# Kernel tuning notes

Hardware: AMD Instinct MI355X
Metric: run time of the kernel (lower is better)

Reference implementation:

```python
import jax, jax.numpy as jnp
import numpy as np

B, T, I = 64, 512, 64
H, O = 256, 64
S, D = 128, 128  # memory_slots == memory_dim (required by the module's update broadcast)


def setup_inputs() -> dict:
    key = jax.random.key(0)
    ks = jax.random.split(key, 12)
    s_ih = 1.0 / np.sqrt(H)
    return {
        "x_seq": jax.random.normal(ks[0], (B, T, I), dtype=jnp.float32),
        # LSTMCell params (torch layout: [4H, I]/[4H, H], gate order i,f,g,o)
        "W_ih": jax.random.uniform(ks[1], (4 * H, I), minval=-s_ih, maxval=s_ih),
        "W_hh": jax.random.uniform(ks[2], (4 * H, H), minval=-s_ih, maxval=s_ih),
        "b_ih": jax.random.uniform(ks[3], (4 * H,), minval=-s_ih, maxval=s_ih),
        "b_hh": jax.random.uniform(ks[4], (4 * H,), minval=-s_ih, maxval=s_ih),
        "W_read": jax.random.normal(ks[5], (D, H)) * 0.02,
        "b_read": jnp.zeros((D,), jnp.float32),
        "W_write": jax.random.normal(ks[6], (D, H)) * 0.02,
        "b_write": jnp.zeros((D,), jnp.float32),
        "W_dec": jax.random.normal(ks[7], (O, H + D)) * 0.02,
        "b_dec": jnpp if False else jnp.zeros((O,), jnp.float32),
    }


def reference(x_seq, W_ih, W_hh, b_ih, b_hh, W_read, b_read, W_write, b_write, W_dec, b_dec):
    def step(carry, x):
        h, c, mem = carry  # h,c: [B,H]; mem: [B,S,D]
        gates = x @ W_ih.T + b_ih + h @ W_hh.T + b_hh  # [B,4H]
        i_g, f_g, g_g, o_g = jnp.split(gates, 4, axis=-1)
        c = jax.nn.sigmoid(f_g) * c + jax.nn.sigmoid(i_g) * jnp.tanh(g_g)
        h = jax.nn.sigmoid(o_g) * jnp.tanh(c)
        # read addressing
        read_keys = h @ W_read.T + b_read                      # [B,D]
        rw = jax.nn.softmax(jnp.einsum('bsd,bd->bs', mem, read_keys), axis=1)
        read_vec = jnp.einsum('bs,bsd->bd', rw, mem)           # [B,D]
        # write addressing + update (add vector = tanh(logits), S == D)
        write_keys = h @ W_write.T + b_write                   # [B,D]
        lw = jnp.einsum('bsd,bd->bs', mem, write_keys)         # [B,S]
        ww = jax.nn.softmax(lw, axis=1)
        add = jnp.tanh(lw)                                     # [B,S] == [B,D]
        mem = mem * (1.0 - ww[:, :, None]) + ww[:, :, None] * add[:, None, :]
        out = jnp.concatenate([h, read_vec], axis=-1) @ W_dec.T + b_dec  # [B,O]
        return (h, c, mem), out

    h0 = jnp.zeros((B, H), x_seq.dtype)
    c0 = jnp.zeros((B, H), x_seq.dtype)
    mem0 = jnp.zeros((B, S, D), x_seq.dtype)  # zero-init buffer, batched after first write
    _, outs = jax.lax.scan(step, (h0, c0, mem0), jnp.swapaxes(x_seq, 0, 1))
    return jnp.swapaxes(outs, 0, 1)  # [B,T,O]
```

## Files before the change

kernel.cpp:

```cpp
#include <hip/hip_runtime.h>


typedef _Float16 f16x2 __attribute__((ext_vector_type(2)));

#define NB   64
#define TT   512
#define RPP  100
#define QRG  25
#define QLD  7
#define XP_BYTES  (67108864u)
#define HD_BYTES  (16777216u)

__device__ unsigned char g_ntm_ws[XP_BYTES + HD_BYTES];

union U32H { unsigned int u; f16x2 h; };
union USH  { _Float16 f; unsigned short u; };
static __device__ __forceinline__ unsigned int pack2f(float a, float b) {
    U32H v; v.h = f16x2{(_Float16)a, (_Float16)b}; return v.u;
}
static __device__ __forceinline__ f16x2 up(unsigned int u) { U32H v; v.u = u; return v.h; }
static __device__ __forceinline__ unsigned short f2s(float a) { USH v; v.f = (_Float16)a; return v.u; }

__device__ __forceinline__ float sigf(float x) { return 1.0f / (1.0f + __expf(-x)); }
__device__ __forceinline__ float tanhfast(float x) {
    float e = __expf(2.0f * x);
    return 1.0f - 2.0f / (e + 1.0f);
}

#if __has_builtin(__builtin_amdgcn_fdot2)
__device__ __forceinline__ float dot2(f16x2 a, f16x2 b, float c) {
    return __builtin_amdgcn_fdot2(a, b, c, false);
}
#else
__device__ __forceinline__ float dot2(f16x2 a, f16x2 b, float c) {
    return c + (float)a.x * (float)b.x + (float)a.y * (float)b.y;
}
#endif

__global__ void __attribute__((amdgpu_flat_work_group_size(512, 512)))
xproj_kernel(const float* __restrict__ x_seq, const float* __restrict__ W_ih,
             const float* __restrict__ b_ih, const float* __restrict__ b_hh,
             unsigned short* XPh)
{
    if (!XPh) XPh = (unsigned short*)g_ntm_ws;
    __shared__ unsigned int xq[128 * 32];
    const int tid = threadIdx.x;
    const int b   = blockIdx.x >> 2;
    const int q   = blockIdx.x & 3;

    {
        const float* src = x_seq + ((size_t)b * TT + (size_t)q * 128 + (tid >> 2)) * 64
                         + (tid & 3) * 16;
        unsigned int* dst = xq + (tid >> 2) * 32 + (tid & 3) * 8;
#pragma unroll
        for (int i = 0; i < 4; ++i) {
            float4 v = ((const float4*)src)[i];
            dst[2 * i]     = pack2f(v.x, v.y);
            dst[2 * i + 1] = pack2f(v.z, v.w);
        }
    }

    unsigned int w0p[32], w1p[32];
    {
        const float* r0 = W_ih + (size_t)tid * 64;
        const float* r1 = W_ih + (size_t)(tid + 512) * 64;
#pragma unroll
        for (int i = 0; i < 16; ++i) {
            float4 v0 = *(const float4*)(r0 + 4 * i);
            float4 v1 = *(const float4*)(r1 + 4 * i);
            w0p[2*i] = pack2f(v0.x, v0.y); w0p[2*i+1] = pack2f(v0.z, v0.w);
            w1p[2*i] = pack2f(v1.x, v1.y); w1p[2*i+1] = pack2f(v1.z, v1.w);
        }
    }
    const float bias0 = b_ih[tid]       + b_hh[tid];
    const float bias1 = b_ih[tid + 512] + b_hh[tid + 512];
    const int   g4A   = (tid & 255) * 4 + ((tid < 256) ? 0 : 1);
    __syncthreads();

    unsigned short* outh = XPh + ((size_t)b * TT + (size_t)q * 128) * 1024;
    for (int tt = 0; tt < 128; ++tt) {
        const uint4* xr = (const uint4*)(xq + tt * 32);
        float a0 = bias0, a1 = bias1;
        float a2 = 0.f, a3 = 0.f, a4 = 0.f, a5 = 0.f, a6 = 0.f, a7 = 0.f;
#pragma unroll
        for (int i = 0; i < 8; ++i) {
            uint4 xv = xr[i];
            a0 = dot2(up(w0p[4*i]),   up(xv.x), a0);  a1 = dot2(up(w1p[4*i]),   up(xv.x), a1);
            a2 = dot2(up(w0p[4*i+1]), up(xv.y), a2);  a3 = dot2(up(w1p[4*i+1]), up(xv.y), a3);
            a4 = dot2(up(w0p[4*i+2]), up(xv.z), a4);  a5 = dot2(up(w1p[4*i+2]), up(xv.z), a5);
            a6 = dot2(up(w0p[4*i+3]), up(xv.w), a6);  a7 = dot2(up(w1p[4*i+3]), up(xv.w), a7);
        }
        const float gA = (a0 + a2) + (a4 + a6);
        const float gB = (a1 + a3) + (a5 + a7);
        outh[tt * 1024 + g4A]     = f2s(gA);
        outh[tt * 1024 + g4A + 2] = f2s(gB);
    }
}

__global__ void
__attribute__((amdgpu_flat_work_group_size(512, 512), amdgpu_waves_per_eu(2, 2),
               amdgpu_num_vgpr(240)))
ntm_rec(const float* __restrict__ W_hh,
        const unsigned short* __restrict__ XPh_in,
        unsigned short* __restrict__ Hd_in)
{
    extern __shared__ char smem[];
    uint4*    wl4 = (uint4*)smem;
    _Float16* h16 = (_Float16*)(smem + 14 * 512 * 16);

    const unsigned short* XPh = XPh_in ? XPh_in : (const unsigned short*)g_ntm_ws;
    unsigned short*       Hd  = Hd_in  ? Hd_in  : (unsigned short*)(g_ntm_ws + XP_BYTES);

    const int tid = threadIdx.x;
    const int b   = blockIdx.x;
    const int u   = tid >> 1;
    const int e   = tid & 1;

    const float* r0 = W_hh + (size_t)(u + 512 * e) * 256;
    const float* r1 = W_hh + (size_t)(256 + u + 512 * e) * 256;

    f16x2 w0[RPP], w1[RPP];
#pragma unroll
    for (int p = 0; p < RPP; ++p) {
        float2 va = *(const float2*)(r0 + 2 * p);
        float2 vb = *(const float2*)(r1 + 2 * p);
        w0[p] = f16x2{(_Float16)va.x, (_Float16)va.y};
        w1[p] = f16x2{(_Float16)vb.x, (_Float16)vb.y};
    }
#pragma unroll
    for (int qq = 0; qq < QLD; ++qq) {
        const float* s0 = r0 + 2 * (RPP + 4 * qq);
        const float* s1 = r1 + 2 * (RPP + 4 * qq);
        wl4[(2 * qq)     * 512 + tid] = make_uint4(pack2f(s0[0], s0[1]), pack2f(s0[2], s0[3]),
                                                   pack2f(s0[4], s0[5]), pack2f(s0[6], s0[7]));
        wl4[(2 * qq + 1) * 512 + tid] = make_uint4(pack2f(s1[0], s1[1]), pack2f(s1[2], s1[3]),
                                                   pack2f(s1[4], s1[5]), pack2f(s1[6], s1[7]));
    }
    if (tid < 64) ((uint4*)h16)[tid] = make_uint4(0u, 0u, 0u, 0u);
    float c_state = 0.f;
    __syncthreads();

    const unsigned int* xpb = (const unsigned int*)XPh + (size_t)b * TT * 512;
    uint4*              Hd4 = (uint4*)Hd + (size_t)b * TT * 32;

    unsigned int xpc = xpb[tid];

    for (int t = 0; t < TT; ++t) {
        const uint4* hq = (const uint4*)(h16 + (t & 1) * 256);
        unsigned int xpn = xpc;
        if (t + 1 < TT) xpn = xpb[(size_t)(t + 1) * 512 + tid];

        float a0 = 0.f, a1 = 0.f, a2 = 0.f, a3 = 0.f;
#pragma unroll
        for (int q = 0; q < QRG; ++q) {
            const uint4 hv = hq[q];
            a0 = dot2(w0[4*q],   up(hv.x), a0);  a2 = dot2(w1[4*q],   up(hv.x), a2);
            a1 = dot2(w0[4*q+1], up(hv.y), a1);  a3 = dot2(w1[4*q+1], up(hv.y), a3);
            a0 = dot2(w0[4*q+2], up(hv.z), a0);  a2 = dot2(w1[4*q+2], up(hv.z), a2);
            a1 = dot2(w0[4*q+3], up(hv.w), a1);  a3 = dot2(w1[4*q+3], up(hv.w), a3);
        }
#pragma unroll
        for (int qq = 0; qq < QLD; ++qq) {
            const uint4 hv = hq[QRG + qq];
            const uint4 wv0 = wl4[(2 * qq)     * 512 + tid];
            const uint4 wv1 = wl4[(2 * qq + 1) * 512 + tid];
            a0 = dot2(up(wv0.x), up(hv.x), a0);  a2 = dot2(up(wv1.x), up(hv.x), a2);
            a1 = dot2(up(wv0.y), up(hv.y), a1);  a3 = dot2(up(wv1.y), up(hv.y), a3);
            a0 = dot2(up(wv0.z), up(hv.z), a0);  a2 = dot2(up(wv1.z), up(hv.z), a2);
            a1 = dot2(up(wv0.w), up(hv.w), a1);  a3 = dot2(up(wv1.w), up(hv.w), a3);
        }
        const f16x2 xg = up(xpc);
        const float gM0 = (a0 + a1) + (float)xg.x;
        const float gM1 = (a2 + a3) + (float)xg.y;
        const float p0 = __shfl_xor(gM0, 1);
        const float p1 = __shfl_xor(gM1, 1);
        const float gi = e ? p0 : gM0;
        const float gf = e ? p1 : gM1;
        const float gg = e ? gM0 : p0;
        const float go = e ? gM1 : p1;
        c_state = sigf(gf) * c_state + sigf(gi) * tanhfast(gg);
        const float hn = sigf(go) * tanhfast(c_state);

        _Float16* hw = h16 + ((t + 1) & 1) * 256;
        if (!e) hw[u] = (_Float16)hn;
        __syncthreads();
        if (tid < 32) Hd4[(size_t)t * 32 + tid] = ((const uint4*)hw)[tid];
        xpc = xpn;
    }
}

__global__ void __attribute__((amdgpu_flat_work_group_size(256, 256)))
dec_kernel(const unsigned short* __restrict__ Hd_in,
           const float* __restrict__ W_dec, const float* __restrict__ b_dec,
           float* __restrict__ out)
{
    const unsigned short* Hd = Hd_in ? Hd_in : (const unsigned short*)(g_ntm_ws + XP_BYTES);
    __shared__ unsigned int wdl[64 * 132];
    __shared__ uint4 ht[32 * 32];

    const int tid = threadIdx.x;
    const int b = blockIdx.x >> 2, q = blockIdx.x & 3;

    for (int idx = tid; idx < 64 * 128; idx += 256) {
        const int o = idx >> 7, pp = idx & 127;
        wdl[o * 132 + pp] = pack2f(W_dec[(size_t)o * 384 + 2 * pp],
                                   W_dec[(size_t)o * 384 + 2 * pp + 1]);
    }
    const int o = tid & 63, tq = tid >> 6;
    const float bd = b_dec[o];
    const uint4* Hdb  = (const uint4*)Hd + ((size_t)b * TT + (size_t)q * 128) * 32;
    float*       outb = out + ((size_t)b * TT + (size_t)q * 128) * 64;

    for (int s = 0; s < 4; ++s) {
        __syncthreads();
#pragma unroll
        for (int i = 0; i < 4; ++i) {
            const int idx = tid + 256 * i;
            ht[idx] = Hdb[s * 1024 + idx];
        }
        __syncthreads();

        float acc[8];
#pragma unroll
        for (int j = 0; j < 8; ++j) acc[j] = 0.f;

#pragma unroll
        for (int c = 0; c < 8; ++c) {
            uint4 w0, w1, w2, w3;
            {
                const unsigned int* wp = wdl + o * 132 + 16 * c;
                w0 = make_uint4(wp[0],  wp[1],  wp[2],  wp[3]);
                w1 = make_uint4(wp[4],  wp[5],  wp[6],  wp[7]);
                w2 = make_uint4(wp[8],  wp[9],  wp[10], wp[11]);
                w3 = make_uint4(wp[12], wp[13], wp[14], wp[15]);
            }
#pragma unroll
            for (int j = 0; j < 8; ++j) {
                const uint4* hr = &ht[(tq * 8 + j) * 32 + 4 * c];
                const uint4 h0 = hr[0], h1 = hr[1], h2 = hr[2], h3 = hr[3];
                float d = acc[j];
                d = dot2(up(w0.x), up(h0.x), d); d = dot2(up(w0.y), up(h0.y), d);
                d = dot2(up(w0.z), up(h0.z), d); d = dot2(up(w0.w), up(h0.w), d);
                d = dot2(up(w1.x), up(h1.x), d); d = dot2(up(w1.y), up(h1.y), d);
                d = dot2(up(w1.z), up(h1.z), d); d = dot2(up(w1.w), up(h1.w), d);
                d = dot2(up(w2.x), up(h2.x), d); d = dot2(up(w2.y), up(h2.y), d);
                d = dot2(up(w2.z), up(h2.z), d); d = dot2(up(w2.w), up(h2.w), d);
                d = dot2(up(w3.x), up(h3.x), d); d = dot2(up(w3.y), up(h3.y), d);
                d = dot2(up(w3.z), up(h3.z), d); d = dot2(up(w3.w), up(h3.w), d);
                acc[j] = d;
            }
        }
#pragma unroll
        for (int j = 0; j < 8; ++j)
            outb[(size_t)(s * 32 + tq * 8 + j) * 64 + o] = acc[j] + bd;
    }
}

extern "C" void kernel_launch(void* const* d_in, const int* in_sizes, int n_in,
                              void* d_out, int out_size, void* d_ws, size_t ws_size,
                              hipStream_t stream) {
    const float* x_seq = (const float*)d_in[0];
    const float* W_ih  = (const float*)d_in[1];
    const float* W_hh  = (const float*)d_in[2];
    const float* b_ih  = (const float*)d_in[3];
    const float* b_hh  = (const float*)d_in[4];
    const float* W_dec = (const float*)d_in[9];
    const float* b_dec = (const float*)d_in[10];
    float* out = (float*)d_out;

    unsigned short* XPh = nullptr;
    unsigned short* Hd  = nullptr;
    if (ws_size >= (size_t)XP_BYTES + HD_BYTES) {
        XPh = (unsigned short*)d_ws;
        Hd  = (unsigned short*)((unsigned char*)d_ws + XP_BYTES);
    }

    hipLaunchKernelGGL(xproj_kernel, dim3(256), dim3(512), 0, stream,
                       x_seq, W_ih, b_ih, b_hh, XPh);

    const size_t smem_rec = (size_t)14 * 512 * 16 + 1024;
    hipFuncSetAttribute((const void*)&ntm_rec,
                        hipFuncAttributeMaxDynamicSharedMemorySize, (int)smem_rec);
    hipLaunchKernelGGL(ntm_rec, dim3(NB), dim3(512), smem_rec, stream,
                       W_hh, XPh, Hd);

    hipLaunchKernelGGL(dec_kernel, dim3(256), dim3(256), 0, stream,
                       Hd, W_dec, b_dec, out);
}
```

Before: 947.2 us.

## Split recurrent W_hh weights across VGPRs, LDS and AGPRs

The recurrent LSTM kernel now keeps 44 packed fp16 weight pairs per row in VGPRs, 36 in LDS and 48 in accumulation registers (AGPRs), written and read back with inline v_accvgpr instructions. Before, the split was 100 in VGPRs and 28 in LDS. The fixed VGPR cap is dropped. The aim is to reduce VGPR pressure and keep more weights resident per step, which cuts the LDS traffic of the per-timestep matvec. The cost is an extra accvgpr read for every AGPR-held weight each step, plus more LDS use.

New measurement: 1.233 ms. +30.2%, slower.

```diff
diff --git a/kernel.cpp b/kernel.cpp
--- a/kernel.cpp
+++ b/kernel.cpp
@@ -5,9 +5,11 @@
 
 #define NB   64
 #define TT   512
-#define RPP  100
-#define QRG  25
-#define QLD  7
+#define RREG 44
+#define QRG  11
+#define QLD  9
+#define QAG  12
+#define NAG  48
 #define XP_BYTES  (67108864u)
 #define HD_BYTES  (16777216u)
 
@@ -98,15 +100,14 @@
 }
 
 __global__ void
-__attribute__((amdgpu_flat_work_group_size(512, 512), amdgpu_waves_per_eu(2, 2),
-               amdgpu_num_vgpr(240)))
+__attribute__((amdgpu_flat_work_group_size(512, 512), amdgpu_waves_per_eu(2, 2)))
 ntm_rec(const float* __restrict__ W_hh,
         const unsigned short* __restrict__ XPh_in,
         unsigned short* __restrict__ Hd_in)
 {
     extern __shared__ char smem[];
     uint4*    wl4 = (uint4*)smem;
-    _Float16* h16 = (_Float16*)(smem + 14 * 512 * 16);
+    _Float16* h16 = (_Float16*)(smem + 18 * 512 * 16);
 
     const unsigned short* XPh = XPh_in ? XPh_in : (const unsigned short*)g_ntm_ws;
     unsigned short*       Hd  = Hd_in  ? Hd_in  : (unsigned short*)(g_ntm_ws + XP_BYTES);
@@ -119,23 +120,34 @@
     const float* r0 = W_hh + (size_t)(u + 512 * e) * 256;
     const float* r1 = W_hh + (size_t)(256 + u + 512 * e) * 256;
 
-    f16x2 w0[RPP], w1[RPP];
-#pragma unroll
-    for (int p = 0; p < RPP; ++p) {
+    f16x2 w0[RREG], w1[RREG];
+#pragma unroll
+    for (int p = 0; p < RREG; ++p) {
         float2 va = *(const float2*)(r0 + 2 * p);
         float2 vb = *(const float2*)(r1 + 2 * p);
         w0[p] = f16x2{(_Float16)va.x, (_Float16)va.y};
         w1[p] = f16x2{(_Float16)vb.x, (_Float16)vb.y};
     }
 #pragma unroll
-    for (int qq = 0; qq < QLD; ++qq) {
-        const float* s0 = r0 + 2 * (RPP + 4 * qq);
-        const float* s1 = r1 + 2 * (RPP + 4 * qq);
-        wl4[(2 * qq)     * 512 + tid] = make_uint4(pack2f(s0[0], s0[1]), pack2f(s0[2], s0[3]),
-                                                   pack2f(s0[4], s0[5]), pack2f(s0[6], s0[7]));
-        wl4[(2 * qq + 1) * 512 + tid] = make_uint4(pack2f(s1[0], s1[1]), pack2f(s1[2], s1[3]),
-                                                   pack2f(s1[4], s1[5]), pack2f(s1[6], s1[7]));
-    }
+    for (int j = 0; j < QLD; ++j) {
+        const float* s0 = r0 + 2 * (RREG + 4 * j);
+        const float* s1 = r1 + 2 * (RREG + 4 * j);
+        wl4[(2 * j)     * 512 + tid] = make_uint4(pack2f(s0[0], s0[1]), pack2f(s0[2], s0[3]),
+                                                  pack2f(s0[4], s0[5]), pack2f(s0[6], s0[7]));
+        wl4[(2 * j + 1) * 512 + tid] = make_uint4(pack2f(s1[0], s1[1]), pack2f(s1[2], s1[3]),
+                                                  pack2f(s1[4], s1[5]), pack2f(s1[6], s1[7]));
+    }
+    unsigned int wagA[NAG], wagB[NAG];
+#pragma unroll
+    for (int p = 0; p < NAG; ++p) {
+        const float* sA = r0 + 160 + 2 * p;
+        const float* sB = r1 + 160 + 2 * p;
+        unsigned int ua = pack2f(sA[0], sA[1]);
+        unsigned int ub = pack2f(sB[0], sB[1]);
+        asm volatile("v_accvgpr_write_b32 %0, %1" : "=a"(wagA[p]) : "v"(ua));
+        asm volatile("v_accvgpr_write_b32 %0, %1" : "=a"(wagB[p]) : "v"(ub));
+    }
+
     if (tid < 64) ((uint4*)h16)[tid] = make_uint4(0u, 0u, 0u, 0u);
     float c_state = 0.f;
     __syncthreads();
@@ -160,14 +172,29 @@
             a1 = dot2(w0[4*q+3], up(hv.w), a1);  a3 = dot2(w1[4*q+3], up(hv.w), a3);
         }
 #pragma unroll
-        for (int qq = 0; qq < QLD; ++qq) {
-            const uint4 hv = hq[QRG + qq];
-            const uint4 wv0 = wl4[(2 * qq)     * 512 + tid];
-            const uint4 wv1 = wl4[(2 * qq + 1) * 512 + tid];
+        for (int j = 0; j < QLD; ++j) {
+            const uint4 hv  = hq[QRG + j];
+            const uint4 wv0 = wl4[(2 * j)     * 512 + tid];
+            const uint4 wv1 = wl4[(2 * j + 1) * 512 + tid];
             a0 = dot2(up(wv0.x), up(hv.x), a0);  a2 = dot2(up(wv1.x), up(hv.x), a2);
             a1 = dot2(up(wv0.y), up(hv.y), a1);  a3 = dot2(up(wv1.y), up(hv.y), a3);
             a0 = dot2(up(wv0.z), up(hv.z), a0);  a2 = dot2(up(wv1.z), up(hv.z), a2);
             a1 = dot2(up(wv0.w), up(hv.w), a1);  a3 = dot2(up(wv1.w), up(hv.w), a3);
+        }
+#pragma unroll
+        for (int j = 0; j < QAG; ++j) {
+            const uint4 hv = hq[QRG + QLD + j];
+#pragma unroll
+            for (int k = 0; k < 4; ++k) {
+                const int idx = 4 * j + k;
+                const unsigned int hp = (k == 0) ? hv.x : (k == 1) ? hv.y
+                                      : (k == 2) ? hv.z : hv.w;
+                unsigned int ta, tb;
+                asm volatile("v_accvgpr_read_b32 %0, %1" : "=v"(ta) : "a"(wagA[idx]));
+                asm volatile("v_accvgpr_read_b32 %0, %1" : "=v"(tb) : "a"(wagB[idx]));
+                if (k & 1) { a1 = dot2(up(ta), up(hp), a1);  a3 = dot2(up(tb), up(hp), a3); }
+                else       { a0 = dot2(up(ta), up(hp), a0);  a2 = dot2(up(tb), up(hp), a2); }
+            }
         }
         const f16x2 xg = up(xpc);
         const float gM0 = (a0 + a1) + (float)xg.x;
@@ -278,7 +305,7 @@
     hipLaunchKernelGGL(xproj_kernel, dim3(256), dim3(512), 0, stream,
                        x_seq, W_ih, b_ih, b_hh, XPh);
 
-    const size_t smem_rec = (size_t)14 * 512 * 16 + 1024;
+    const size_t smem_rec = (size_t)18 * 512 * 16 + 1024;
     hipFuncSetAttribute((const void*)&ntm_rec,
                         hipFuncAttributeMaxDynamicSharedMemorySize, (int)smem_rec);
     hipLaunchKernelGGL(ntm_rec, dim3(NB), dim3(512), smem_rec, stream,
```

## Stream most W_hh slices from a prepacked global buffer instead of registers

Applied to the files above, without the earlier changes.

Adds a pack kernel that converts the upper part of W_hh to fp16 in a global workspace buffer laid out per thread. The recurrent kernel now keeps only 20 pairs of weight registers and 18 uint4 slices in LDS, and reads the remaining 36 slices from global memory (L2-resident) on every timestep. This cuts register pressure (the VGPR cap is removed) at the cost of per-step global loads on the latency-critical serial recurrence.

Result: slower. 1.878 ms (+98.2%).

```diff
diff --git a/kernel.cpp b/kernel.cpp
--- a/kernel.cpp
+++ b/kernel.cpp
@@ -5,13 +5,11 @@
 
 #define NB   64
 #define TT   512
-#define RPP  100
-#define QRG  25
-#define QLD  7
 #define XP_BYTES  (67108864u)
 #define HD_BYTES  (16777216u)
-
-__device__ unsigned char g_ntm_ws[XP_BYTES + HD_BYTES];
+#define WS_BYTES  (294912u)
+
+__device__ unsigned char g_ntm_ws[XP_BYTES + HD_BYTES + WS_BYTES];
 
 union U32H { unsigned int u; f16x2 h; };
 union USH  { _Float16 f; unsigned short u; };
@@ -36,6 +34,22 @@
     return c + (float)a.x * (float)b.x + (float)a.y * (float)b.y;
 }
 #endif
+
+__global__ void __attribute__((amdgpu_flat_work_group_size(512, 512)))
+pack_kernel(const float* __restrict__ W_hh, unsigned int* WSu)
+{
+    if (!WSu) WSu = (unsigned int*)(g_ntm_ws + XP_BYTES + HD_BYTES);
+    const int s   = blockIdx.x;
+    const int tid = threadIdx.x;
+    const int u = tid >> 1, e = tid & 1;
+    const int row = (s & 1) ? (256 + u + 512 * e) : (u + 512 * e);
+    const int qA  = 14 + (s >> 1);
+    const float* rp = W_hh + (size_t)row * 256 + 8 * qA;
+    uint4 v;
+    v.x = pack2f(rp[0], rp[1]); v.y = pack2f(rp[2], rp[3]);
+    v.z = pack2f(rp[4], rp[5]); v.w = pack2f(rp[6], rp[7]);
+    ((uint4*)WSu)[s * 512 + tid] = v;
+}
 
 __global__ void __attribute__((amdgpu_flat_work_group_size(512, 512)))
 xproj_kernel(const float* __restrict__ x_seq, const float* __restrict__ W_ih,
@@ -98,18 +112,20 @@
 }
 
 __global__ void
-__attribute__((amdgpu_flat_work_group_size(512, 512), amdgpu_waves_per_eu(2, 2),
-               amdgpu_num_vgpr(240)))
+__attribute__((amdgpu_flat_work_group_size(512, 512), amdgpu_waves_per_eu(2, 2)))
 ntm_rec(const float* __restrict__ W_hh,
         const unsigned short* __restrict__ XPh_in,
-        unsigned short* __restrict__ Hd_in)
+        unsigned short* __restrict__ Hd_in,
+        const unsigned int* __restrict__ WS_in)
 {
     extern __shared__ char smem[];
     uint4*    wl4 = (uint4*)smem;
-    _Float16* h16 = (_Float16*)(smem + 14 * 512 * 16);
+    _Float16* h16 = (_Float16*)(smem + 18 * 512 * 16);
 
     const unsigned short* XPh = XPh_in ? XPh_in : (const unsigned short*)g_ntm_ws;
     unsigned short*       Hd  = Hd_in  ? Hd_in  : (unsigned short*)(g_ntm_ws + XP_BYTES);
+    const uint4*          WSq = (const uint4*)(WS_in ? WS_in
+                              : (const unsigned int*)(g_ntm_ws + XP_BYTES + HD_BYTES));
 
     const int tid = threadIdx.x;
     const int b   = blockIdx.x;
@@ -119,23 +135,24 @@
     const float* r0 = W_hh + (size_t)(u + 512 * e) * 256;
     const float* r1 = W_hh + (size_t)(256 + u + 512 * e) * 256;
 
-    f16x2 w0[RPP], w1[RPP];
-#pragma unroll
-    for (int p = 0; p < RPP; ++p) {
+    f16x2 w0[20], w1[20];
+#pragma unroll
+    for (int p = 0; p < 20; ++p) {
         float2 va = *(const float2*)(r0 + 2 * p);
         float2 vb = *(const float2*)(r1 + 2 * p);
         w0[p] = f16x2{(_Float16)va.x, (_Float16)va.y};
         w1[p] = f16x2{(_Float16)vb.x, (_Float16)vb.y};
     }
 #pragma unroll
-    for (int qq = 0; qq < QLD; ++qq) {
-        const float* s0 = r0 + 2 * (RPP + 4 * qq);
-        const float* s1 = r1 + 2 * (RPP + 4 * qq);
-        wl4[(2 * qq)     * 512 + tid] = make_uint4(pack2f(s0[0], s0[1]), pack2f(s0[2], s0[3]),
-                                                   pack2f(s0[4], s0[5]), pack2f(s0[6], s0[7]));
-        wl4[(2 * qq + 1) * 512 + tid] = make_uint4(pack2f(s1[0], s1[1]), pack2f(s1[2], s1[3]),
-                                                   pack2f(s1[4], s1[5]), pack2f(s1[6], s1[7]));
-    }
+    for (int j = 0; j < 9; ++j) {
+        const float* s0 = r0 + 40 + 8 * j;
+        const float* s1 = r1 + 40 + 8 * j;
+        wl4[(2 * j)     * 512 + tid] = make_uint4(pack2f(s0[0], s0[1]), pack2f(s0[2], s0[3]),
+                                                  pack2f(s0[4], s0[5]), pack2f(s0[6], s0[7]));
+        wl4[(2 * j + 1) * 512 + tid] = make_uint4(pack2f(s1[0], s1[1]), pack2f(s1[2], s1[3]),
+                                                  pack2f(s1[4], s1[5]), pack2f(s1[6], s1[7]));
+    }
+
     if (tid < 64) ((uint4*)h16)[tid] = make_uint4(0u, 0u, 0u, 0u);
     float c_state = 0.f;
     __syncthreads();
@@ -151,24 +168,36 @@
         if (t + 1 < TT) xpn = xpb[(size_t)(t + 1) * 512 + tid];
 
         float a0 = 0.f, a1 = 0.f, a2 = 0.f, a3 = 0.f;
-#pragma unroll
-        for (int q = 0; q < QRG; ++q) {
+
+#pragma unroll
+        for (int j = 0; j < 18; ++j) {
+            const uint4 hv  = hq[14 + j];
+            const uint4 wsa = WSq[(2 * j)     * 512 + tid];
+            const uint4 wsb = WSq[(2 * j + 1) * 512 + tid];
+            a0 = dot2(up(wsa.x), up(hv.x), a0);  a2 = dot2(up(wsb.x), up(hv.x), a2);
+            a1 = dot2(up(wsa.y), up(hv.y), a1);  a3 = dot2(up(wsb.y), up(hv.y), a3);
+            a0 = dot2(up(wsa.z), up(hv.z), a0);  a2 = dot2(up(wsb.z), up(hv.z), a2);
+            a1 = dot2(up(wsa.w), up(hv.w), a1);  a3 = dot2(up(wsb.w), up(hv.w), a3);
+        }
+#pragma unroll
+        for (int j = 0; j < 9; ++j) {
+            const uint4 hv  = hq[5 + j];
+            const uint4 wv0 = wl4[(2 * j)     * 512 + tid];
+            const uint4 wv1 = wl4[(2 * j + 1) * 512 + tid];
+            a0 = dot2(up(wv0.x), up(hv.x), a0);  a2 = dot2(up(wv1.x), up(hv.x), a2);
+            a1 = dot2(up(wv0.y), up(hv.y), a1);  a3 = dot2(up(wv1.y), up(hv.y), a3);
+            a0 = dot2(up(wv0.z), up(hv.z), a0);  a2 = dot2(up(wv1.z), up(hv.z), a2);
+            a1 = dot2(up(wv0.w), up(hv.w), a1);  a3 = dot2(up(wv1.w), up(hv.w), a3);
+        }
+#pragma unroll
+        for (int q = 0; q < 5; ++q) {
             const uint4 hv = hq[q];
             a0 = dot2(w0[4*q],   up(hv.x), a0);  a2 = dot2(w1[4*q],   up(hv.x), a2);
             a1 = dot2(w0[4*q+1], up(hv.y), a1);  a3 = dot2(w1[4*q+1], up(hv.y), a3);
             a0 = dot2(w0[4*q+2], up(hv.z), a0);  a2 = dot2(w1[4*q+2], up(hv.z), a2);
             a1 = dot2(w0[4*q+3], up(hv.w), a1);  a3 = dot2(w1[4*q+3], up(hv.w), a3);
         }
-#pragma unroll
-        for (int qq = 0; qq < QLD; ++qq) {
-            const uint4 hv = hq[QRG + qq];
-            const uint4 wv0 = wl4[(2 * qq)     * 512 + tid];
-            const uint4 wv1 = wl4[(2 * qq + 1) * 512 + tid];
-            a0 = dot2(up(wv0.x), up(hv.x), a0);  a2 = dot2(up(wv1.x), up(hv.x), a2);
-            a1 = dot2(up(wv0.y), up(hv.y), a1);  a3 = dot2(up(wv1.y), up(hv.y), a3);
-            a0 = dot2(up(wv0.z), up(hv.z), a0);  a2 = dot2(up(wv1.z), up(hv.z), a2);
-            a1 = dot2(up(wv0.w), up(hv.w), a1);  a3 = dot2(up(wv1.w), up(hv.w), a3);
-        }
+
         const f16x2 xg = up(xpc);
         const float gM0 = (a0 + a1) + (float)xg.x;
         const float gM1 = (a2 + a3) + (float)xg.y;
@@ -270,19 +299,22 @@
 
     unsigned short* XPh = nullptr;
     unsigned short* Hd  = nullptr;
-    if (ws_size >= (size_t)XP_BYTES + HD_BYTES) {
+    unsigned int*   WS  = nullptr;
+    if (ws_size >= (size_t)XP_BYTES + HD_BYTES + WS_BYTES) {
         XPh = (unsigned short*)d_ws;
         Hd  = (unsigned short*)((unsigned char*)d_ws + XP_BYTES);
-    }
-
+        WS  = (unsigned int*)((unsigned char*)d_ws + XP_BYTES + HD_BYTES);
+    }
+
+    hipLaunchKernelGGL(pack_kernel, dim3(36), dim3(512), 0, stream, W_hh, WS);
     hipLaunchKernelGGL(xproj_kernel, dim3(256), dim3(512), 0, stream,
                        x_seq, W_ih, b_ih, b_hh, XPh);
 
-    const size_t smem_rec = (size_t)14 * 512 * 16 + 1024;
+    const size_t smem_rec = (size_t)18 * 512 * 16 + 1024;
     hipFuncSetAttribute((const void*)&ntm_rec,
                         hipFuncAttributeMaxDynamicSharedMemorySize, (int)smem_rec);
     hipLaunchKernelGGL(ntm_rec, dim3(NB), dim3(512), smem_rec, stream,
-                       W_hh, XPh, Hd);
+                       W_hh, XPh, Hd, WS);
 
     hipLaunchKernelGGL(dec_kernel, dim3(256), dim3(256), 0, stream,
                        Hd, W_dec, b_dec, out);
```
